# Optimization experiments

Hardware: AMD Instinct MI355X
Metric: run time of the kernel (lower is better)

The kernel has to match this reference:

```python
import jax, jax.numpy as jnp
import numpy as np

N = 8192        # nodes
E = 49152       # edges (~avg degree 6, triangular mesh)
H = 6           # GATv2 heads
C = 512         # hidden_size (per-head out channels)
F_IN = 2 + C    # GATv2 in_channels = coord(2) + hidden(512)
ALL_FEAT = 37   # deform_in_c-2 + 16 + 16
NUM_LOOP = 3
LRELU_SLOPE = 0.2


def setup_inputs() -> dict:
    key = jax.random.key(0)
    ks = jax.random.split(key, 10)
    x = jax.random.uniform(ks[0], (N, 7), dtype=jnp.float32)
    local_feat = jax.random.normal(ks[1], (N, 16), dtype=jnp.float32)
    conv_feat = jax.random.normal(ks[2], (N, 16), dtype=jnp.float32)
    edge_index = jax.random.randint(ks[3], (2, E), 0, N, dtype=jnp.int64)
    bd_mask = jnp.zeros((N,), jnp.int32)  # poly_mesh=False path
    W_lin = jax.random.normal(ks[4], (ALL_FEAT, C), dtype=jnp.float32) / np.float32(np.sqrt(ALL_FEAT))
    b_lin = jnp.zeros((C,), jnp.float32)
    Wl = jax.random.normal(ks[5], (F_IN, H * C), dtype=jnp.float32) / np.float32(np.sqrt(F_IN))
    Wr = jax.random.normal(ks[6], (F_IN, H * C), dtype=jnp.float32) / np.float32(np.sqrt(F_IN))
    att = jax.random.normal(ks[7], (H, C), dtype=jnp.float32) / np.float32(np.sqrt(C))
    gat_bias = jnp.zeros((C,), jnp.float32)
    W_coord = jax.random.normal(ks[8], (C, 2), dtype=jnp.float32) / np.float32(np.sqrt(C))
    b_coord = jnp.zeros((2,), jnp.float32)
    return dict(x=x, local_feat=local_feat, conv_feat=conv_feat,
                W_lin=W_lin, b_lin=b_lin, Wl=Wl, Wr=Wr, att=att,
                gat_bias=gat_bias, W_coord=W_coord, b_coord=b_coord,
                edge_index=edge_index, bd_mask=bd_mask)


def _gatv2(feat, src, dst, Wl, Wr, att, bias):
    # PyG GATv2Conv: lin_l on source, lin_r on target, additive attention
    n = feat.shape[0]
    xl = (feat @ Wl).reshape(n, H, C)            # source-side transform
    xr = (feat @ Wr).reshape(n, H, C)            # target-side transform
    e = xl[src] + xr[dst]                        # [E', H, C]
    e = jax.nn.leaky_relu(e, LRELU_SLOPE)
    logits = jnp.einsum('ehc,hc->eh', e, att)    # [E', H]
    m = jax.ops.segment_max(logits, dst, num_segments=n)
    m = jnp.where(jnp.isfinite(m), m, 0.0)
    a = jnp.exp(logits - m[dst])
    denom = jax.ops.segment_sum(a, dst, num_segments=n) + 1e-16
    alpha = a / denom[dst]                       # segment softmax over incoming edges
    msg = xl[src] * alpha[:, :, None]            # [E', H, C]
    out = jax.ops.segment_sum(msg, dst, num_segments=n)  # [N, H, C]
    return out.mean(axis=1) + bias               # concat=False -> mean over heads


def reference(x, local_feat, conv_feat, W_lin, b_lin, Wl, Wr, att, gat_bias,
              W_coord, b_coord, edge_index, bd_mask):
    coord = x[:, :2]
    hidden_in = jnp.concatenate([x[:, 2:], local_feat, conv_feat], axis=1)
    hidden = jax.nn.selu(hidden_in @ W_lin + b_lin)
    # GATv2Conv adds self-loops by default
    loops = jnp.arange(N, dtype=edge_index.dtype)
    src = jnp.concatenate([edge_index[0], loops])
    dst = jnp.concatenate([edge_index[1], loops])
    for _ in range(NUM_LOOP):
        up = coord[:, 0] == 1.0
        down = coord[:, 0] == 0.0
        left = coord[:, 1] == 0.0
        right = coord[:, 1] == 1.0
        feat = jnp.concatenate([coord, hidden], axis=1)   # [N, 514]
        hidden = jax.nn.selu(_gatv2(feat, src, dst, Wl, Wr, att, gat_bias))
        out = hidden @ W_coord + b_coord                  # [N, 2]
        ox = jnp.where(down, 0.0, jnp.where(up, 1.0, out[:, 0]))
        oy = jnp.where(right, 1.0, jnp.where(left, 0.0, out[:, 1]))
        coord = jnp.stack([ox, oy], axis=1)
    return coord
```

## Files before the change

kernel.cpp:

```cpp
#include <hip/hip_runtime.h>
#include <hip/hip_bf16.h>
#include <math.h>

#define N_NODES   8192
#define NUM_E     49152
#define NUM_EDGES (NUM_E + N_NODES)
#define H_HEADS   6
#define C_DIM     512
#define HC        (H_HEADS * C_DIM)
#define XLR       (2 * HC)
#define N_FEAT    37
#define LRELU_SLOPE 0.2f
#define SELU_LAMBDA 1.0507009873554805f
#define SELU_ALPHA  1.6732632423543772f

typedef __bf16 bf16_t;
typedef bf16_t bf16x8 __attribute__((ext_vector_type(8)));
typedef float  f32x4  __attribute__((ext_vector_type(4)));
typedef float  f32x2  __attribute__((ext_vector_type(2)));

__device__ __forceinline__ int edge_src(const int* ei, int e) {
    return e < NUM_E ? ei[e] : (e - NUM_E);
}
__device__ __forceinline__ int edge_dst(const int* ei, int e) {
    return e < NUM_E ? ei[NUM_E + e] : (e - NUM_E);
}
__device__ __forceinline__ float selu_f(float v) {
    return v > 0.f ? SELU_LAMBDA * v : SELU_LAMBDA * SELU_ALPHA * (__expf(v) - 1.f);
}
__device__ __forceinline__ void gload_lds16(const void* g, void* l) {
    __builtin_amdgcn_global_load_lds((const __attribute__((address_space(1))) void*)g,
                                     (__attribute__((address_space(3))) void*)l, 16, 0, 0);
}

__global__ __launch_bounds__(512) void k_hidden0(
    const float* __restrict__ x, const float* __restrict__ lf,
    const float* __restrict__ cf, const float* __restrict__ W,
    const float* __restrict__ b, bf16_t* __restrict__ hidden,
    float* __restrict__ coord)
{
    int n = blockIdx.x;
    int c = threadIdx.x;
    __shared__ float f[N_FEAT];
    if (c < 5)            f[c] = x[n*7 + 2 + c];
    else if (c < 21)      f[c] = lf[n*16 + (c-5)];
    else if (c < N_FEAT)  f[c] = cf[n*16 + (c-21)];
    if (c < 2) coord[n*2 + c] = x[n*7 + c];
    __syncthreads();
    float acc = b[c];
    #pragma unroll
    for (int k = 0; k < N_FEAT; ++k) acc = fmaf(f[k], W[k*C_DIM + c], acc);
    hidden[n*C_DIM + c] = (bf16_t)selu_f(acc);
}

__global__ __launch_bounds__(256) void k_wt_transpose(const float* __restrict__ W,
                                                      bf16_t* __restrict__ WT)
{
    __shared__ float tile[32][33];
    int k0 = blockIdx.y * 32;
    int n0 = blockIdx.x * 32;
    int tx = threadIdx.x & 31, ty = threadIdx.x >> 5;
    #pragma unroll
    for (int i = 0; i < 4; ++i)
        tile[ty + i*8][tx] = W[(size_t)(k0 + 2 + ty + i*8) * HC + n0 + tx];
    __syncthreads();
    #pragma unroll
    for (int i = 0; i < 4; ++i)
        WT[(size_t)(n0 + ty + i*8) * C_DIM + k0 + tx] = (bf16_t)tile[tx][ty + i*8];
}

__global__ void k_hist(const int* __restrict__ ei, int* __restrict__ counts) {
    int e = blockIdx.x * blockDim.x + threadIdx.x;
    if (e >= NUM_EDGES) return;
    atomicAdd(&counts[edge_dst(ei, e)], 1);
}

__global__ __launch_bounds__(256) void k_scan(const int* __restrict__ counts,
                                              int* __restrict__ row_ptr,
                                              int* __restrict__ cursor) {
    __shared__ int part[256];
    __shared__ int off[257];
    int t = threadIdx.x;
    int base = t * 32;
    int local[32];
    int s = 0;
    #pragma unroll
    for (int i = 0; i < 32; ++i) { local[i] = s; s += counts[base + i]; }
    part[t] = s;
    __syncthreads();
    if (t == 0) {
        off[0] = 0;
        for (int i = 0; i < 256; ++i) off[i+1] = off[i] + part[i];
    }
    __syncthreads();
    int o = off[t];
    #pragma unroll
    for (int i = 0; i < 32; ++i) {
        int v = o + local[i];
        row_ptr[base + i] = v;
        cursor[base + i]  = v;
    }
    if (t == 255) row_ptr[N_NODES] = off[256];
}

__global__ void k_scatter(const int* __restrict__ ei, int* __restrict__ cursor,
                          int* __restrict__ csr_eid) {
    int e = blockIdx.x * blockDim.x + threadIdx.x;
    if (e >= NUM_EDGES) return;
    int pos = atomicAdd(&cursor[edge_dst(ei, e)], 1);
    csr_eid[pos] = e;
}

#define BM 256
#define BN 256
#define BK 64
#define NT (C_DIM / BK)
#define NBX (XLR / BN)
#define NWG ((N_NODES / BM) * NBX)

__global__ __launch_bounds__(512, 2) void k_gemm_bf16(
    const bf16_t* __restrict__ A,
    const bf16_t* __restrict__ BT,
    const float*  __restrict__ Wl,
    const float*  __restrict__ Wr,
    const float*  __restrict__ coord,
    bf16_t* __restrict__ out)
{
    __shared__ __align__(1024) char smem[131072];
    char* sA = smem;
    char* sB = smem + 65536;

    const int tid  = threadIdx.x;
    const int wave = tid >> 6;
    const int lane = tid & 63;
    const int wm   = wave >> 2;
    const int wn   = wave & 3;

    int bid = blockIdx.y * gridDim.x + blockIdx.x;
    bid = (bid & 7) * (NWG / 8) + (bid >> 3);
    const int rowBase = (bid / NBX) * BM;
    const int colBase = (bid % NBX) * BN;

    const int rtid = tid >> 3;
    const int csw  = ((tid & 7) * 8) ^ (((tid >> 3) & 7) << 3);
    const bf16_t* pA = A  + (size_t)(rowBase + rtid) * C_DIM + csw;
    const bf16_t* pB = BT + (size_t)(colBase + rtid) * C_DIM + csw;

    auto stageA = [&](int t, int h) {
        char* l = sA + ((t & 1) << 15) + (h << 14) + (wave << 10);
        const bf16_t* g = pA + (size_t)(h * 128) * C_DIM + t * BK;
        gload_lds16(g,              l);
        gload_lds16(g + 64 * C_DIM, l + 8192);
    };
    auto stageB = [&](int t, int h) {
        char* l = sB + ((t & 1) << 15) + (h << 14) + (wave << 10);
        const bf16_t* g = pB + (size_t)(h * 128) * C_DIM + t * BK;
        gload_lds16(g,              l);
        gload_lds16(g + 64 * C_DIM, l + 8192);
    };

    stageB(0, 0); stageB(0, 1); stageA(0, 0); stageA(0, 1);
    stageB(1, 0); stageB(1, 1);
    __builtin_amdgcn_sched_barrier(0);
    asm volatile("s_waitcnt vmcnt(4)" ::: "memory");
    __builtin_amdgcn_sched_barrier(0);
    __builtin_amdgcn_s_barrier();
    __builtin_amdgcn_sched_barrier(0);

    const int kb  = (lane >> 4) << 4;
    const int sw  = (lane & 7) << 4;
    const int xt0 = kb ^ sw;
    const int xt1 = (64 | kb) ^ sw;
    const int aRowOff = (wm * 128 + (lane & 15)) * 128;
    const int bRowOff = (wn * 64  + (lane & 15)) * 128;

    f32x4 acc[8][4] = {};

    #pragma unroll 2
    for (int t = 0; t < NT; ++t) {
        const char* aP = sA + ((t & 1) << 15) + aRowOff;
        const char* bP = sB + ((t & 1) << 15) + bRowOff;
        bf16x8 bfv[4][2];

        #pragma unroll
        for (int ph = 0; ph < 4; ++ph) {
            if (ph == 0)      { if (t + 1 < NT) stageA(t + 1, 0); }
            else if (ph == 1) { if (t + 1 < NT) stageA(t + 1, 1); }
            else if (ph == 2) { if (t + 2 < NT) stageB(t + 2, 0); }
            else              { if (t + 2 < NT) stageB(t + 2, 1); }

            if (ph == 0) {
                #pragma unroll
                for (int nf = 0; nf < 4; ++nf) {
                    bfv[nf][0] = *(const bf16x8*)(bP + nf * 2048 + xt0);
                    bfv[nf][1] = *(const bf16x8*)(bP + nf * 2048 + xt1);
                }
            }
            bf16x8 af0k0 = *(const bf16x8*)(aP + (2*ph)     * 2048 + xt0);
            bf16x8 af0k1 = *(const bf16x8*)(aP + (2*ph)     * 2048 + xt1);
            bf16x8 af1k0 = *(const bf16x8*)(aP + (2*ph + 1) * 2048 + xt0);
            bf16x8 af1k1 = *(const bf16x8*)(aP + (2*ph + 1) * 2048 + xt1);

            __builtin_amdgcn_s_setprio(1);
            #pragma unroll
            for (int nf = 0; nf < 4; ++nf) {
                acc[2*ph  ][nf] = __builtin_amdgcn_mfma_f32_16x16x32_bf16(af0k0, bfv[nf][0], acc[2*ph  ][nf], 0, 0, 0);
                acc[2*ph+1][nf] = __builtin_amdgcn_mfma_f32_16x16x32_bf16(af1k0, bfv[nf][0], acc[2*ph+1][nf], 0, 0, 0);
            }
            #pragma unroll
            for (int nf = 0; nf < 4; ++nf) {
                acc[2*ph  ][nf] = __builtin_amdgcn_mfma_f32_16x16x32_bf16(af0k1, bfv[nf][1], acc[2*ph  ][nf], 0, 0, 0);
                acc[2*ph+1][nf] = __builtin_amdgcn_mfma_f32_16x16x32_bf16(af1k1, bfv[nf][1], acc[2*ph+1][nf], 0, 0, 0);
            }
            __builtin_amdgcn_s_setprio(0);

            if (ph == 3) {
                __builtin_amdgcn_sched_barrier(0);
                if (t < NT - 2)       asm volatile("s_waitcnt vmcnt(4)" ::: "memory");
                else if (t == NT - 2) asm volatile("s_waitcnt vmcnt(0)" ::: "memory");
            }
            __builtin_amdgcn_sched_barrier(0);
            asm volatile("s_waitcnt lgkmcnt(0)" ::: "memory");
            __builtin_amdgcn_s_barrier();
            __builtin_amdgcn_sched_barrier(0);
        }
    }

    const float* Wtop = (colBase < HC) ? Wl : Wr;
    const int coff = (colBase < HC) ? 0 : HC;
    const int ccol  = lane & 15;
    const int crow4 = (lane >> 4) * 4;

    float wv0[4], wv1[4];
    #pragma unroll
    for (int nf = 0; nf < 4; ++nf) {
        int wcol = colBase + wn*64 + nf*16 + ccol - coff;
        wv0[nf] = Wtop[wcol];
        wv1[nf] = Wtop[HC + wcol];
    }
    #pragma unroll
    for (int mf = 0; mf < 8; ++mf) {
        #pragma unroll
        for (int r = 0; r < 4; ++r) {
            int row = rowBase + wm*128 + mf*16 + crow4 + r;
            float c0 = coord[row*2 + 0], c1 = coord[row*2 + 1];
            size_t rb = (size_t)row * XLR;
            #pragma unroll
            for (int nf = 0; nf < 4; ++nf) {
                int col = colBase + wn*64 + nf*16 + ccol;
                out[rb + col] = (bf16_t)(acc[mf][nf][r] + c0 * wv0[nf] + c1 * wv1[nf]);
            }
        }
    }
}

#define MAX_DEG 128
__global__ __launch_bounds__(384) void k_attn_agg(
    const bf16_t* __restrict__ xlr,
    const int* __restrict__ row_ptr, const int* __restrict__ csr_eid,
    const int* __restrict__ ei, const float* __restrict__ att,
    const float* __restrict__ gat_bias, const float* __restrict__ W_coord,
    const float* __restrict__ b_coord, const float* __restrict__ coord_in,
    bf16_t* __restrict__ hidden, float* __restrict__ coord_out)
{
    int n = blockIdx.x;
    int tid = threadIdx.x;
    int h = tid >> 6, lane = tid & 63;
    __shared__ int   s_src[MAX_DEG + 2];
    __shared__ float s_acc[HC];
    __shared__ float s_red[12];

    int beg = row_ptr[n];
    int deg = min(row_ptr[n + 1] - beg, MAX_DEG);
    int degR = (deg + 1) & ~1;
    for (int j = tid; j < degR + 2; j += 384)
        s_src[j] = (j < deg) ? edge_src(ei, csr_eid[beg + j]) : n;
    __syncthreads();

    size_t off = (size_t)h * C_DIM + lane * 8;
    bf16x8 xrv = *(const bf16x8*)(xlr + (size_t)n * XLR + HC + off);
    f32x2 xr2[4], at2[4], ac2[4] = {};
    #pragma unroll
    for (int i = 0; i < 4; ++i) {
        xr2[i] = f32x2{(float)xrv[2*i], (float)xrv[2*i+1]};
        at2[i] = f32x2{att[off + 2*i], att[off + 2*i + 1]};
    }

    float l = 0.f;
    bf16x8 xa = *(const bf16x8*)(xlr + (size_t)s_src[0] * XLR + off);
    bf16x8 xb = *(const bf16x8*)(xlr + (size_t)s_src[1] * XLR + off);
    for (int j = 0; j < degR; j += 2) {
        bf16x8 na = *(const bf16x8*)(xlr + (size_t)s_src[j + 2] * XLR + off);
        bf16x8 nb = *(const bf16x8*)(xlr + (size_t)s_src[j + 3] * XLR + off);

        f32x2 xla[4], xlb[4];
        #pragma unroll
        for (int i = 0; i < 4; ++i) {
            xla[i] = f32x2{(float)xa[2*i], (float)xa[2*i+1]};
            xlb[i] = f32x2{(float)xb[2*i], (float)xb[2*i+1]};
        }
        f32x2 sa = {0.f, 0.f}, sb = {0.f, 0.f};
        #pragma unroll
        for (int i = 0; i < 4; ++i) {
            f32x2 va = xla[i] + xr2[i];
            f32x2 vb = xlb[i] + xr2[i];
            sa += __builtin_elementwise_max(va, va * LRELU_SLOPE) * at2[i];
            sb += __builtin_elementwise_max(vb, vb * LRELU_SLOPE) * at2[i];
        }
        float suma = sa.x + sa.y, sumb = sb.x + sb.y;
        #pragma unroll
        for (int o = 1; o < 64; o <<= 1) {
            suma += __shfl_xor(suma, o);
            sumb += __shfl_xor(sumb, o);
        }
        float aa = __expf(suma);
        float ab = __expf(sumb);
        ab = (j + 1 < deg) ? ab : 0.f;
        l += aa + ab;
        #pragma unroll
        for (int i = 0; i < 4; ++i) ac2[i] += aa * xla[i] + ab * xlb[i];

        xa = na; xb = nb;
    }

    float invl = 1.f / (l + 1e-16f) * (1.f / 6.f);
    #pragma unroll
    for (int i = 0; i < 4; ++i) {
        s_acc[off + 2*i]     = ac2[i].x * invl;
        s_acc[off + 2*i + 1] = ac2[i].y * invl;
    }
    __syncthreads();

    float p0 = 0.f, p1 = 0.f;
    for (int c = tid; c < C_DIM; c += 384) {
        float s = 0.f;
        #pragma unroll
        for (int hh = 0; hh < H_HEADS; ++hh) s += s_acc[hh * C_DIM + c];
        float hv = selu_f(s + gat_bias[c]);
        hidden[n * C_DIM + c] = (bf16_t)hv;
        p0 = fmaf(hv, W_coord[c * 2 + 0], p0);
        p1 = fmaf(hv, W_coord[c * 2 + 1], p1);
    }
    #pragma unroll
    for (int o = 32; o > 0; o >>= 1) { p0 += __shfl_down(p0, o); p1 += __shfl_down(p1, o); }
    if (lane == 0) { s_red[h * 2] = p0; s_red[h * 2 + 1] = p1; }
    __syncthreads();
    if (tid == 0) {
        float o0 = b_coord[0], o1 = b_coord[1];
        #pragma unroll
        for (int w = 0; w < H_HEADS; ++w) { o0 += s_red[w * 2]; o1 += s_red[w * 2 + 1]; }
        float cx = coord_in[n * 2 + 0], cy = coord_in[n * 2 + 1];
        float ox = (cx == 0.0f) ? 0.f : ((cx == 1.0f) ? 1.f : o0);
        float oy = (cy == 1.0f) ? 1.f : ((cy == 0.0f) ? 0.f : o1);
        coord_out[n * 2 + 0] = ox;
        coord_out[n * 2 + 1] = oy;
    }
}

extern "C" void kernel_launch(void* const* d_in, const int* in_sizes, int n_in,
                              void* d_out, int out_size, void* d_ws, size_t ws_size,
                              hipStream_t stream)
{
    const float* x       = (const float*)d_in[0];
    const float* lf      = (const float*)d_in[1];
    const float* cf      = (const float*)d_in[2];
    const float* W_lin   = (const float*)d_in[3];
    const float* b_lin   = (const float*)d_in[4];
    const float* Wl      = (const float*)d_in[5];
    const float* Wr      = (const float*)d_in[6];
    const float* att     = (const float*)d_in[7];
    const float* gbias   = (const float*)d_in[8];
    const float* W_coord = (const float*)d_in[9];
    const float* b_coord = (const float*)d_in[10];
    const int*   ei      = (const int*)d_in[11];

    char* w = (char*)d_ws;
    auto alloc = [&](size_t bytes) { char* p = w; w += (bytes + 255) & ~255ull; return p; };
    bf16_t*   hidden  = (bf16_t*)alloc((size_t)N_NODES * C_DIM * 2);
    bf16_t*   WT      = (bf16_t*)alloc((size_t)XLR * C_DIM * 2);
    bf16_t*   xlr     = (bf16_t*)alloc((size_t)N_NODES * XLR * 2);
    int*      counts  = (int*)alloc((size_t)N_NODES * 4);
    int*      row_ptr = (int*)alloc((size_t)(N_NODES + 1) * 4);
    int*      cursor  = (int*)alloc((size_t)N_NODES * 4);
    int*      csr_eid = (int*)alloc((size_t)NUM_EDGES * 4);
    float*    cA      = (float*)alloc((size_t)N_NODES * 2 * 4);
    float*    cB      = (float*)alloc((size_t)N_NODES * 2 * 4);

    hipMemsetAsync(counts, 0, (size_t)N_NODES * 4, stream);
    k_hidden0<<<N_NODES, 512, 0, stream>>>(x, lf, cf, W_lin, b_lin, hidden, cA);
    {
        dim3 tg(HC / 32, C_DIM / 32);
        k_wt_transpose<<<tg, 256, 0, stream>>>(Wl, WT);
        k_wt_transpose<<<tg, 256, 0, stream>>>(Wr, WT + (size_t)HC * C_DIM);
    }
    k_hist<<<(NUM_EDGES + 255) / 256, 256, 0, stream>>>(ei, counts);
    k_scan<<<1, 256, 0, stream>>>(counts, row_ptr, cursor);
    k_scatter<<<(NUM_EDGES + 255) / 256, 256, 0, stream>>>(ei, cursor, csr_eid);

    float* cin = cA;
    for (int it = 0; it < 3; ++it) {
        float* cout = (it == 2) ? (float*)d_out : ((it == 0) ? cB : cA);
        dim3 g(NBX, N_NODES / BM);
        k_gemm_bf16<<<g, 512, 0, stream>>>(hidden, WT, Wl, Wr, cin, xlr);
        k_attn_agg<<<N_NODES, 384, 0, stream>>>(xlr, row_ptr, csr_eid, ei, att,
                                                gbias, W_coord, b_coord, cin, hidden, cout);
        cin = cout;
    }
}
```

Measured before the change: 577.6 us.

## Make attention kernel persistent with next-node prefetch and store CSR source ids

The CSR scatter now stores the source node index directly instead of the edge id, which removes one dependent lookup per neighbour. The attention/aggregation kernel becomes a persistent kernel on a fixed grid of 1280 blocks that strides over nodes. While it works on the current node, it prefetches the next node's row pointers, neighbour list and target-side features. The in-loop double-buffered neighbour loads are dropped, and odd-degree padding is now masked by a very negative logit; the CSR buffer is zero-padded so fixed-width reads stay in bounds. The aim is to cut block launch overhead and hide the index-fetch latency, at the cost of less per-edge prefetching and lower parallelism per node.

```diff
diff --git a/kernel.cpp b/kernel.cpp
--- a/kernel.cpp
+++ b/kernel.cpp
@@ -104,11 +104,11 @@
 }
 
 __global__ void k_scatter(const int* __restrict__ ei, int* __restrict__ cursor,
-                          int* __restrict__ csr_eid) {
+                          int* __restrict__ csr_src) {
     int e = blockIdx.x * blockDim.x + threadIdx.x;
     if (e >= NUM_EDGES) return;
     int pos = atomicAdd(&cursor[edge_dst(ei, e)], 1);
-    csr_eid[pos] = e;
+    csr_src[pos] = edge_src(ei, e);
 }
 
 #define BM 256
@@ -255,105 +255,123 @@
 }
 
 #define MAX_DEG 128
+#define GRID_P  1280
 __global__ __launch_bounds__(384) void k_attn_agg(
     const bf16_t* __restrict__ xlr,
-    const int* __restrict__ row_ptr, const int* __restrict__ csr_eid,
-    const int* __restrict__ ei, const float* __restrict__ att,
+    const int* __restrict__ row_ptr, const int* __restrict__ csr_src,
+    const float* __restrict__ att,
     const float* __restrict__ gat_bias, const float* __restrict__ W_coord,
     const float* __restrict__ b_coord, const float* __restrict__ coord_in,
     bf16_t* __restrict__ hidden, float* __restrict__ coord_out)
 {
-    int n = blockIdx.x;
     int tid = threadIdx.x;
     int h = tid >> 6, lane = tid & 63;
-    __shared__ int   s_src[MAX_DEG + 2];
+    __shared__ int   s_src[MAX_DEG];
     __shared__ float s_acc[HC];
     __shared__ float s_red[12];
 
-    int beg = row_ptr[n];
-    int deg = min(row_ptr[n + 1] - beg, MAX_DEG);
-    int degR = (deg + 1) & ~1;
-    for (int j = tid; j < degR + 2; j += 384)
-        s_src[j] = (j < deg) ? edge_src(ei, csr_eid[beg + j]) : n;
+    size_t off = (size_t)h * C_DIM + lane * 8;
+    f32x2 at2[4];
+    #pragma unroll
+    for (int i = 0; i < 4; ++i)
+        at2[i] = f32x2{att[off + 2*i], att[off + 2*i + 1]};
+
+    int n   = blockIdx.x;
+    int beg = row_ptr[n], end = row_ptr[n + 1];
+    int deg = min(end - beg, MAX_DEG);
+    if (tid < MAX_DEG) s_src[tid] = csr_src[beg + tid];
+    bf16x8 xrv = *(const bf16x8*)(xlr + (size_t)n * XLR + HC + off);
+
+    int nxt = n + GRID_P;
+    int begN = 0, endN = 0, v_src = 0;
+    if (nxt < N_NODES) { begN = row_ptr[nxt]; endN = row_ptr[nxt + 1]; }
     __syncthreads();
-
-    size_t off = (size_t)h * C_DIM + lane * 8;
-    bf16x8 xrv = *(const bf16x8*)(xlr + (size_t)n * XLR + HC + off);
-    f32x2 xr2[4], at2[4], ac2[4] = {};
-    #pragma unroll
-    for (int i = 0; i < 4; ++i) {
-        xr2[i] = f32x2{(float)xrv[2*i], (float)xrv[2*i+1]};
-        at2[i] = f32x2{att[off + 2*i], att[off + 2*i + 1]};
-    }
-
-    float l = 0.f;
-    bf16x8 xa = *(const bf16x8*)(xlr + (size_t)s_src[0] * XLR + off);
-    bf16x8 xb = *(const bf16x8*)(xlr + (size_t)s_src[1] * XLR + off);
-    for (int j = 0; j < degR; j += 2) {
-        bf16x8 na = *(const bf16x8*)(xlr + (size_t)s_src[j + 2] * XLR + off);
-        bf16x8 nb = *(const bf16x8*)(xlr + (size_t)s_src[j + 3] * XLR + off);
-
-        f32x2 xla[4], xlb[4];
+    if (nxt < N_NODES && tid < MAX_DEG) v_src = csr_src[begN + tid];
+
+    while (true) {
+        bf16x8 xrv_nxt = {};
+        if (nxt < N_NODES)
+            xrv_nxt = *(const bf16x8*)(xlr + (size_t)nxt * XLR + HC + off);
+
+        f32x2 xr2[4], ac2[4] = {};
+        #pragma unroll
+        for (int i = 0; i < 4; ++i)
+            xr2[i] = f32x2{(float)xrv[2*i], (float)xrv[2*i+1]};
+
+        int degR = (deg + 1) & ~1;
+        float l = 0.f;
+        for (int j = 0; j < degR; j += 2) {
+            bf16x8 xa = *(const bf16x8*)(xlr + (size_t)s_src[j]     * XLR + off);
+            bf16x8 xb = *(const bf16x8*)(xlr + (size_t)s_src[j + 1] * XLR + off);
+            f32x2 xla[4], xlb[4];
+            #pragma unroll
+            for (int i = 0; i < 4; ++i) {
+                xla[i] = f32x2{(float)xa[2*i], (float)xa[2*i+1]};
+                xlb[i] = f32x2{(float)xb[2*i], (float)xb[2*i+1]};
+            }
+            f32x2 sa = {0.f, 0.f}, sb = {0.f, 0.f};
+            #pragma unroll
+            for (int i = 0; i < 4; ++i) {
+                f32x2 va = xla[i] + xr2[i];
+                f32x2 vb = xlb[i] + xr2[i];
+                sa += __builtin_elementwise_max(va, va * LRELU_SLOPE) * at2[i];
+                sb += __builtin_elementwise_max(vb, vb * LRELU_SLOPE) * at2[i];
+            }
+            float suma = sa.x + sa.y, sumb = sb.x + sb.y;
+            #pragma unroll
+            for (int o = 1; o < 64; o <<= 1) {
+                suma += __shfl_xor(suma, o);
+                sumb += __shfl_xor(sumb, o);
+            }
+            sumb = (j + 1 < deg) ? sumb : -1e30f;
+            float aa = __expf(suma), ab = __expf(sumb);
+            l += aa + ab;
+            #pragma unroll
+            for (int i = 0; i < 4; ++i) ac2[i] += aa * xla[i] + ab * xlb[i];
+        }
+
+        float invl = 1.f / (l + 1e-16f) * (1.f / 6.f);
         #pragma unroll
         for (int i = 0; i < 4; ++i) {
-            xla[i] = f32x2{(float)xa[2*i], (float)xa[2*i+1]};
-            xlb[i] = f32x2{(float)xb[2*i], (float)xb[2*i+1]};
-        }
-        f32x2 sa = {0.f, 0.f}, sb = {0.f, 0.f};
+            s_acc[off + 2*i]     = ac2[i].x * invl;
+            s_acc[off + 2*i + 1] = ac2[i].y * invl;
+        }
+        __syncthreads();
+
+        if (nxt < N_NODES && tid < MAX_DEG) s_src[tid] = v_src;
+        int nxt2 = nxt + GRID_P;
+        int begN2 = 0, endN2 = 0;
+        if (nxt2 < N_NODES) { begN2 = row_ptr[nxt2]; endN2 = row_ptr[nxt2 + 1]; }
+
+        float p0 = 0.f, p1 = 0.f;
+        for (int c = tid; c < C_DIM; c += 384) {
+            float s = 0.f;
+            #pragma unroll
+            for (int hh = 0; hh < H_HEADS; ++hh) s += s_acc[hh * C_DIM + c];
+            float hv = selu_f(s + gat_bias[c]);
+            hidden[n * C_DIM + c] = (bf16_t)hv;
+            p0 = fmaf(hv, W_coord[c * 2 + 0], p0);
+            p1 = fmaf(hv, W_coord[c * 2 + 1], p1);
+        }
         #pragma unroll
-        for (int i = 0; i < 4; ++i) {
-            f32x2 va = xla[i] + xr2[i];
-            f32x2 vb = xlb[i] + xr2[i];
-            sa += __builtin_elementwise_max(va, va * LRELU_SLOPE) * at2[i];
-            sb += __builtin_elementwise_max(vb, vb * LRELU_SLOPE) * at2[i];
-        }
-        float suma = sa.x + sa.y, sumb = sb.x + sb.y;
-        #pragma unroll
-        for (int o = 1; o < 64; o <<= 1) {
-            suma += __shfl_xor(suma, o);
-            sumb += __shfl_xor(sumb, o);
-        }
-        float aa = __expf(suma);
-        float ab = __expf(sumb);
-        ab = (j + 1 < deg) ? ab : 0.f;
-        l += aa + ab;
-        #pragma unroll
-        for (int i = 0; i < 4; ++i) ac2[i] += aa * xla[i] + ab * xlb[i];
-
-        xa = na; xb = nb;
-    }
-
-    float invl = 1.f / (l + 1e-16f) * (1.f / 6.f);
-    #pragma unroll
-    for (int i = 0; i < 4; ++i) {
-        s_acc[off + 2*i]     = ac2[i].x * invl;
-        s_acc[off + 2*i + 1] = ac2[i].y * invl;
-    }
-    __syncthreads();
-
-    float p0 = 0.f, p1 = 0.f;
-    for (int c = tid; c < C_DIM; c += 384) {
-        float s = 0.f;
-        #pragma unroll
-        for (int hh = 0; hh < H_HEADS; ++hh) s += s_acc[hh * C_DIM + c];
-        float hv = selu_f(s + gat_bias[c]);
-        hidden[n * C_DIM + c] = (bf16_t)hv;
-        p0 = fmaf(hv, W_coord[c * 2 + 0], p0);
-        p1 = fmaf(hv, W_coord[c * 2 + 1], p1);
-    }
-    #pragma unroll
-    for (int o = 32; o > 0; o >>= 1) { p0 += __shfl_down(p0, o); p1 += __shfl_down(p1, o); }
-    if (lane == 0) { s_red[h * 2] = p0; s_red[h * 2 + 1] = p1; }
-    __syncthreads();
-    if (tid == 0) {
-        float o0 = b_coord[0], o1 = b_coord[1];
-        #pragma unroll
-        for (int w = 0; w < H_HEADS; ++w) { o0 += s_red[w * 2]; o1 += s_red[w * 2 + 1]; }
-        float cx = coord_in[n * 2 + 0], cy = coord_in[n * 2 + 1];
-        float ox = (cx == 0.0f) ? 0.f : ((cx == 1.0f) ? 1.f : o0);
-        float oy = (cy == 1.0f) ? 1.f : ((cy == 0.0f) ? 0.f : o1);
-        coord_out[n * 2 + 0] = ox;
-        coord_out[n * 2 + 1] = oy;
+        for (int o = 32; o > 0; o >>= 1) { p0 += __shfl_down(p0, o); p1 += __shfl_down(p1, o); }
+        if (lane == 0) { s_red[h * 2] = p0; s_red[h * 2 + 1] = p1; }
+        __syncthreads();
+        if (tid == 0) {
+            float o0 = b_coord[0], o1 = b_coord[1];
+            #pragma unroll
+            for (int w = 0; w < H_HEADS; ++w) { o0 += s_red[w * 2]; o1 += s_red[w * 2 + 1]; }
+            float cx = coord_in[n * 2 + 0], cy = coord_in[n * 2 + 1];
+            float ox = (cx == 0.0f) ? 0.f : ((cx == 1.0f) ? 1.f : o0);
+            float oy = (cy == 1.0f) ? 1.f : ((cy == 0.0f) ? 0.f : o1);
+            coord_out[n * 2 + 0] = ox;
+            coord_out[n * 2 + 1] = oy;
+        }
+
+        if (nxt >= N_NODES) break;
+        n = nxt; deg = min(endN - begN, MAX_DEG); xrv = xrv_nxt;
+        nxt = nxt2; begN = begN2; endN = endN2;
+        if (nxt < N_NODES && tid < MAX_DEG) v_src = csr_src[begN + tid];
     }
 }
 
@@ -382,11 +400,12 @@
     int*      counts  = (int*)alloc((size_t)N_NODES * 4);
     int*      row_ptr = (int*)alloc((size_t)(N_NODES + 1) * 4);
     int*      cursor  = (int*)alloc((size_t)N_NODES * 4);
-    int*      csr_eid = (int*)alloc((size_t)NUM_EDGES * 4);
+    int*      csr_src = (int*)alloc((size_t)(NUM_EDGES + MAX_DEG) * 4);
     float*    cA      = (float*)alloc((size_t)N_NODES * 2 * 4);
     float*    cB      = (float*)alloc((size_t)N_NODES * 2 * 4);
 
     hipMemsetAsync(counts, 0, (size_t)N_NODES * 4, stream);
+    hipMemsetAsync(csr_src + NUM_EDGES, 0, (size_t)MAX_DEG * 4, stream);
     k_hidden0<<<N_NODES, 512, 0, stream>>>(x, lf, cf, W_lin, b_lin, hidden, cA);
     {
         dim3 tg(HC / 32, C_DIM / 32);
@@ -395,15 +414,15 @@
     }
     k_hist<<<(NUM_EDGES + 255) / 256, 256, 0, stream>>>(ei, counts);
     k_scan<<<1, 256, 0, stream>>>(counts, row_ptr, cursor);
-    k_scatter<<<(NUM_EDGES + 255) / 256, 256, 0, stream>>>(ei, cursor, csr_eid);
+    k_scatter<<<(NUM_EDGES + 255) / 256, 256, 0, stream>>>(ei, cursor, csr_src);
 
     float* cin = cA;
     for (int it = 0; it < 3; ++it) {
         float* cout = (it == 2) ? (float*)d_out : ((it == 0) ? cB : cA);
         dim3 g(NBX, N_NODES / BM);
         k_gemm_bf16<<<g, 512, 0, stream>>>(hidden, WT, Wl, Wr, cin, xlr);
-        k_attn_agg<<<N_NODES, 384, 0, stream>>>(xlr, row_ptr, csr_eid, ei, att,
-                                                gbias, W_coord, b_coord, cin, hidden, cout);
+        k_attn_agg<<<GRID_P, 384, 0, stream>>>(xlr, row_ptr, csr_src, att,
+                                               gbias, W_coord, b_coord, cin, hidden, cout);
         cin = cout;
     }
 }
```

Result: slower. 633.6 us (+9.7%).
